# Kernel tuning notes

Hardware: AMD Instinct MI355X
Metric: run time of the kernel (lower is better)

The kernel has to match this reference:

```python
import jax, jax.numpy as jnp
import numpy as np

NTOKEN = 32000
NHID = 1024
BATCH = 64
LEAVES = 256          # leaves per balanced binary tree
SEQLEN = 768          # 3*LEAVES-2 = 766, padded to 768
MAX_DEPTH = 64        # stack bound; balanced tree needs ~log2(LEAVES)+2
OPEN, CLOSE = 0, 1
PAD = NTOKEN - 1


def _build_tree(rng, n_leaves):
    # "( left right )" encoding: open, subtrees, close; leaf ids in [2, NTOKEN-2]
    if n_leaves == 1:
        return [int(rng.integers(2, NTOKEN - 1))]
    l = n_leaves // 2
    return [OPEN] + _build_tree(rng, l) + _build_tree(rng, n_leaves - l) + [CLOSE]


def setup_inputs() -> dict:
    rng = np.random.default_rng(0)
    seqs = []
    for _ in range(BATCH):
        s = _build_tree(rng, LEAVES)
        s = s + [PAD] * (SEQLEN - len(s))
        seqs.append(s)
    tokens = jnp.asarray(np.asarray(seqs, dtype=np.int32).T)  # [S, B]

    key = jax.random.key(0)
    k1, k2 = jax.random.split(key, 2)
    emb = jax.random.normal(k1, (NTOKEN, NHID), jnp.float32) * 0.1
    emb = emb.at[PAD].set(0.0)  # padding_idx row is zero
    W = jax.random.normal(k2, (NHID, 2 * NHID), jnp.float32) * (1.0 / np.sqrt(2 * NHID))
    b = jnp.zeros((NHID,), jnp.float32)
    return {"tokens": tokens, "emb": emb, "W": W, "b": b}


def _parse_all(tokens, emb, W, b):
    # tokens: [S, B] int32. Shift-reduce stack machine, scanned over sequence,
    # vmapped over batch. Dropout is 0 (eval / default), so op = tanh(Linear).
    nhid = emb.shape[1]

    def parse_one(toks):  # toks: [S]
        stack0 = jnp.zeros((MAX_DEPTH, nhid), emb.dtype)

        def step(carry, idx):
            stack, ptr = carry
            is_close = idx == CLOSE
            is_open = idx == OPEN
            is_pad = idx == PAD
            left = stack[ptr - 2]
            right = stack[ptr - 1]
            combined = jnp.tanh(jnp.concatenate([left, right]) @ W.T + b)  # [nhid]
            leaf = emb[idx]
            push = jnp.where(is_close, combined, leaf)
            pos = jnp.where(is_close, ptr - 2, ptr)
            write = jnp.logical_not(is_open | is_pad)
            stack = stack.at[pos].set(jnp.where(write, push, stack[pos]))
            ptr = ptr + jnp.where(is_close, jnp.int32(-1),
                                  jnp.where(write, jnp.int32(1), jnp.int32(0)))
            return (stack, ptr), None

        (stack, _), _ = jax.lax.scan(step, (stack0, jnp.int32(0)), toks)
        return stack[0]  # root representation

    return jax.vmap(parse_one)(tokens.T)  # [B, nhid]


def reference(tokens, emb, W, b):
    return _parse_all(tokens, emb, W, b)
```

## Files before the change

kernel.cpp:

```cpp
#include <hip/hip_runtime.h>

#define B 64
#define SLEN 768
#define NHID 1024
#define K2 2048
#define NTOK 32000
#define PADTOK (NTOK-1)
#define MAXL 16
#define MAXN 256
#define NINT 256
#define STKD 14

typedef unsigned short u16;
typedef unsigned int u32;
typedef __attribute__((ext_vector_type(8))) short short8;
typedef __attribute__((ext_vector_type(4))) float f32x4;

__device__ __forceinline__ u16 f2b(float f) {
  union { float f; u32 i; } v; v.f = f;
  u32 x = v.i;
  return (u16)((x + 0x7FFFu + ((x >> 16) & 1u)) >> 16);
}
__device__ __forceinline__ float fast_tanh(float x) {
  float t = __expf(2.0f * x);
  return 1.0f - 2.0f / (t + 1.0f);
}
__device__ __forceinline__ void glds16(const void* g, void* l) {
  __builtin_amdgcn_global_load_lds(
      (const __attribute__((address_space(1))) void*)g,
      (__attribute__((address_space(3))) void*)l, 16, 0, 0);
}

__global__ void parse_wconv(const int* __restrict__ tokens,
                            const float* __restrict__ W,
                            int* __restrict__ cnt,
                            int* __restrict__ rootArr,
                            int* __restrict__ nNodes,
                            int* __restrict__ LeafTok,
                            int4* __restrict__ flat,
                            u16* __restrict__ Wbf) {
  if (blockIdx.x == 0) {
    int b = threadIdx.x;
    if (b >= B) return;
    int stk[STKD];
#pragma unroll
    for (int i = 0; i < STKD; ++i) stk[i] = 0;
    int nint = 0, leafc = 0;
    for (int t0 = 0; t0 < SLEN; t0 += 32) {
      int v[32];
#pragma unroll
      for (int i = 0; i < 32; ++i) v[i] = tokens[(t0 + i) * B + b];
#pragma unroll
      for (int i = 0; i < 32; ++i) {
        int idx = v[i];
        if (idx == 1) {
          int t1 = stk[0], t2 = stk[1];
          int l1 = (t1 >> 16) & 15, l2 = (t2 >> 16) & 15;
          int lvl = (l1 > l2 ? l1 : l2) + 1;
          if (lvl > 15) lvl = 15;
          if (nint < NINT)
            flat[b * NINT + nint] = make_int4(t2 & 0x4000FFFF, t1 & 0x4000FFFF, lvl, 0);
#pragma unroll
          for (int j = 1; j < STKD - 1; ++j) stk[j] = stk[j + 1];
          stk[0] = (lvl << 16) | nint;
          ++nint;
        } else if (idx != 0 && idx != PADTOK) {
          int slot = (leafc < 256) ? leafc : 255;
          LeafTok[b * 256 + slot] = idx;
          ++leafc;
#pragma unroll
          for (int j = STKD - 1; j > 0; --j) stk[j] = stk[j - 1];
          stk[0] = 0x40000000 | slot;
        }
      }
    }
    rootArr[b] = stk[0] & 0x4000FFFF;
    nNodes[b] = (nint < NINT) ? nint : NINT;
    cnt[b * MAXL + 0] = (leafc < 256) ? leafc : 256;
  } else {
    int id = (blockIdx.x - 1) * 256 + threadIdx.x;
    int stride = (gridDim.x - 1) * 256;
    for (int i = id; i < (NHID * K2) / 4; i += stride) {
      float4 v = reinterpret_cast<const float4*>(W)[i];
      ushort4 o = {f2b(v.x), f2b(v.y), f2b(v.z), f2b(v.w)};
      reinterpret_cast<ushort4*>(Wbf)[i] = o;
    }
  }
}

__global__ void bucket_leaf(const float* __restrict__ emb,
                            const int* __restrict__ LeafTok,
                            int* __restrict__ cnt,
                            const int* __restrict__ nNodes,
                            const int4* __restrict__ flat,
                            int4* __restrict__ nodes,
                            u16* __restrict__ LeafVals) {
  int bid = blockIdx.x;
  if (bid < B) {
    int i = threadIdx.x;
    if (i < nNodes[bid]) {
      int4 r = flat[bid * NINT + i];
      int slot = atomicAdd(&cnt[bid * MAXL + r.z], 1);
      if (slot < MAXN)
        nodes[((size_t)(bid * MAXL + r.z)) * MAXN + slot] = make_int4(r.x, r.y, i, 0);
    }
  } else {
    int r = bid - B;
    int b = r >> 8, slot = r & 255;
    if (slot < cnt[b * MAXL + 0]) {
      int tok = LeafTok[b * 256 + slot];
      const float* src = emb + (size_t)tok * NHID;
      u16* dst = LeafVals + ((size_t)(b * 256 + slot)) * NHID;
      int t = threadIdx.x * 4;
      float4 v = *reinterpret_cast<const float4*>(src + t);
      ushort4 o = {f2b(v.x), f2b(v.y), f2b(v.z), f2b(v.w)};
      *reinterpret_cast<ushort4*>(dst + t) = o;
    }
  }
}

__launch_bounds__(256, 3)
__global__ void combine_mfma(const u16* __restrict__ Wbf,
                             const float* __restrict__ bias,
                             const int* __restrict__ cnt,
                             const int4* __restrict__ nodes,
                             const int* __restrict__ rootArr,
                             const u16* __restrict__ LeafVals,
                             u16* __restrict__ Vals,
                             float* __restrict__ out,
                             int level) {
  __shared__ short As[8192];
  __shared__ short Bs[8192];
  __shared__ const u16* sL[128];
  __shared__ const u16* sR[128];
  __shared__ int sOut[128];
  __shared__ int sRoot[128];

  int cnt0 = cnt[level];
  if (cnt0 <= 0) return;
  int rowsTotal = B * cnt0;
  int mTiles = (rowsTotal + 127) >> 7;
  int totalTiles = mTiles * 8;
  int tid = threadIdx.x;
  int lane = tid & 63, wave = tid >> 6;
  int wm = wave & 1, wn = wave >> 1;

  for (int tile = blockIdx.x; tile < totalTiles; tile += gridDim.x) {
    int mt = tile >> 3, nt = tile & 7;
    int m0 = mt << 7, n0 = nt << 7;
    __syncthreads();
    if (tid < 128) {
      int r = m0 + tid;
      const u16* lp = Wbf; const u16* rp = Wbf; int ov = -1, rf = -1;
      if (r < rowsTotal) {
        int bb = r / cnt0, j = r - bb * cnt0;
        if (j < cnt[bb * MAXL + level]) {
          int4 rec = nodes[((size_t)(bb * MAXL + level)) * MAXN + j];
          int lr = rec.x, rr = rec.y;
          lp = (lr & 0x40000000) ? LeafVals + (size_t)(bb * 256 + (lr & 0xFFFF)) * NHID
                                 : Vals + ((size_t)bb * NINT + lr) * NHID;
          rp = (rr & 0x40000000) ? LeafVals + (size_t)(bb * 256 + (rr & 0xFFFF)) * NHID
                                 : Vals + ((size_t)bb * NINT + rr) * NHID;
          ov = bb * NINT + rec.z;
          int rt = rootArr[bb];
          if (!(rt & 0x40000000) && rec.z == rt) rf = bb * NHID;
        }
      }
      sL[tid] = lp; sR[tid] = rp; sOut[tid] = ov; sRoot[tid] = rf;
    }
    __syncthreads();

    int kq = (tid & 3) * 8;
    const u16* a0L = sL[tid >> 2] + kq;      const u16* a0R = sR[tid >> 2] + kq;
    const u16* a1L = sL[64 + (tid >> 2)] + kq; const u16* a1R = sR[64 + (tid >> 2)] + kq;
    const u16* b0 = Wbf + (size_t)(n0 + (tid >> 2)) * K2 + kq;
    const u16* b1 = Wbf + (size_t)(n0 + 64 + (tid >> 2)) * K2 + kq;
    short* AsW = As + wave * 512;
    short* BsW = Bs + wave * 512;

    f32x4 acc[4][4];
#pragma unroll
    for (int i = 0; i < 4; ++i)
#pragma unroll
      for (int j = 0; j < 4; ++j) acc[i][j] = {0.f, 0.f, 0.f, 0.f};

    int aBase = (wm * 64 + (lane & 15)) * 32 + (lane >> 4) * 8;
    int bBase = (wn * 64 + (lane & 15)) * 32 + (lane >> 4) * 8;

    for (int k0 = 0; k0 < K2; k0 += 64) {
#pragma unroll
      for (int p = 0; p < 2; ++p) {
        int k = k0 + p * 32;
        const u16* sa0 = (k < NHID) ? (a0L + k) : (a0R + (k - NHID));
        const u16* sa1 = (k < NHID) ? (a1L + k) : (a1R + (k - NHID));
        glds16(sa0, AsW + p * 4096);
        glds16(sa1, AsW + p * 4096 + 2048);
        glds16(b0 + k, BsW + p * 4096);
        glds16(b1 + k, BsW + p * 4096 + 2048);
      }
      __syncthreads();
#pragma unroll
      for (int p = 0; p < 2; ++p) {
        short8 af[4], bw[4];
#pragma unroll
        for (int mi = 0; mi < 4; ++mi)
          af[mi] = *reinterpret_cast<const short8*>(As + p * 4096 + aBase + mi * 512);
#pragma unroll
        for (int ni = 0; ni < 4; ++ni)
          bw[ni] = *reinterpret_cast<const short8*>(Bs + p * 4096 + bBase + ni * 512);
#pragma unroll
        for (int mi = 0; mi < 4; ++mi)
#pragma unroll
          for (int ni = 0; ni < 4; ++ni)
            acc[mi][ni] = __builtin_amdgcn_mfma_f32_16x16x32_bf16(
                af[mi], bw[ni], acc[mi][ni], 0, 0, 0);
      }
      __syncthreads();
    }

#pragma unroll
    for (int ni = 0; ni < 4; ++ni) {
      int n = n0 + wn * 64 + ni * 16 + (lane & 15);
      float bv = bias[n];
#pragma unroll
      for (int mi = 0; mi < 4; ++mi) {
#pragma unroll
        for (int reg = 0; reg < 4; ++reg) {
          int mloc = wm * 64 + mi * 16 + (lane >> 4) * 4 + reg;
          int ov = sOut[mloc];
          if (ov >= 0) {
            float v = fast_tanh(acc[mi][ni][reg] + bv);
            Vals[(size_t)ov * NHID + n] = f2b(v);
            int rf = sRoot[mloc];
            if (rf >= 0) out[rf + n] = v;
          }
        }
      }
    }
  }
}

extern "C" void kernel_launch(void* const* d_in, const int* in_sizes, int n_in,
                              void* d_out, int out_size, void* d_ws, size_t ws_size,
                              hipStream_t stream) {
  const int* tokens = (const int*)d_in[0];
  const float* emb  = (const float*)d_in[1];
  const float* W    = (const float*)d_in[2];
  const float* bias = (const float*)d_in[3];
  float* out = (float*)d_out;

  char* ws = (char*)d_ws;
  int* cnt      = (int*)ws;
  int* rootArr  = (int*)(ws + 4096);
  int* nNodes   = (int*)(ws + 4352);
  int* LeafTok  = (int*)(ws + 8192);
  int4* flat    = (int4*)(ws + 73728);
  int4* nodes   = (int4*)(ws + 335872);
  u16* Wbf      = (u16*)(ws + 4530176);
  u16* LeafVals = (u16*)(ws + 8724480);
  u16* Vals     = (u16*)(ws + 42278912);

  hipMemsetAsync(cnt, 0, 4096, stream);
  parse_wconv<<<65, 256, 0, stream>>>(tokens, W, cnt, rootArr, nNodes,
                                      LeafTok, flat, Wbf);
  bucket_leaf<<<B + B * 256, 256, 0, stream>>>(emb, LeafTok, cnt, nNodes,
                                               flat, nodes, LeafVals);
  for (int L = 1; L <= 9; ++L) {
    int expRows = B * (L <= 8 ? (256 >> L) : 1);
    int mT = (expRows + 127) / 128;
    int grid = mT * 8;
    combine_mfma<<<grid, 256, 0, stream>>>(Wbf, bias, cnt, nodes, rootArr,
                                           LeafVals, Vals, out, L);
  }
}
```

Baseline: 721.2 us.

## Bucket nodes by level during serial parse, drop memset and atomic bucketing pass

```diff
diff --git a/kernel.cpp b/kernel.cpp
--- a/kernel.cpp
+++ b/kernel.cpp
@@ -9,10 +9,10 @@
 #define MAXL 16
 #define MAXN 256
 #define NINT 256
-#define STKD 14
 
 typedef unsigned short u16;
 typedef unsigned int u32;
+typedef unsigned long long u64;
 typedef __attribute__((ext_vector_type(8))) short short8;
 typedef __attribute__((ext_vector_type(4))) float f32x4;
 
@@ -31,52 +31,62 @@
       (__attribute__((address_space(3))) void*)l, 16, 0, 0);
 }
 
+#define PUSH(NEW) do { s11=s10;s10=s9;s9=s8;s8=s7;s7=s6;s6=s5;s5=s4;s4=s3;s3=s2;s2=s1;s1=s0;s0=(NEW); } while(0)
+#define POP2PUSH(NEW) do { s0=(NEW);s1=s2;s2=s3;s3=s4;s4=s5;s5=s6;s6=s7;s7=s8;s8=s9;s9=s10;s10=s11; } while(0)
+
 __global__ void parse_wconv(const int* __restrict__ tokens,
                             const float* __restrict__ W,
                             int* __restrict__ cnt,
                             int* __restrict__ rootArr,
-                            int* __restrict__ nNodes,
                             int* __restrict__ LeafTok,
-                            int4* __restrict__ flat,
+                            int4* __restrict__ nodes,
                             u16* __restrict__ Wbf) {
   if (blockIdx.x == 0) {
     int b = threadIdx.x;
     if (b >= B) return;
-    int stk[STKD];
-#pragma unroll
-    for (int i = 0; i < STKD; ++i) stk[i] = 0;
+    int s0=0,s1=0,s2=0,s3=0,s4=0,s5=0,s6=0,s7=0,s8=0,s9=0,s10=0,s11=0;
+    u64 cA = 0, cB = 0;
     int nint = 0, leafc = 0;
-    for (int t0 = 0; t0 < SLEN; t0 += 32) {
-      int v[32];
-#pragma unroll
-      for (int i = 0; i < 32; ++i) v[i] = tokens[(t0 + i) * B + b];
-#pragma unroll
-      for (int i = 0; i < 32; ++i) {
+    for (int t0 = 0; t0 < SLEN; t0 += 16) {
+      int v[16];
+#pragma unroll
+      for (int i = 0; i < 16; ++i) v[i] = tokens[(t0 + i) * B + b];
+#pragma unroll
+      for (int i = 0; i < 16; ++i) {
         int idx = v[i];
         if (idx == 1) {
-          int t1 = stk[0], t2 = stk[1];
-          int l1 = (t1 >> 16) & 15, l2 = (t2 >> 16) & 15;
+          int l1 = (s0 >> 16) & 15, l2 = (s1 >> 16) & 15;
           int lvl = (l1 > l2 ? l1 : l2) + 1;
           if (lvl > 15) lvl = 15;
+          int slot;
+          if (lvl <= 8) {
+            int sh = (lvl - 1) * 8;
+            slot = (int)((cA >> sh) & 0xFF); cA += 1ull << sh;
+          } else {
+            int sh = (lvl - 9) * 8;
+            slot = (int)((cB >> sh) & 0xFF); cB += 1ull << sh;
+          }
           if (nint < NINT)
-            flat[b * NINT + nint] = make_int4(t2 & 0x4000FFFF, t1 & 0x4000FFFF, lvl, 0);
-#pragma unroll
-          for (int j = 1; j < STKD - 1; ++j) stk[j] = stk[j + 1];
-          stk[0] = (lvl << 16) | nint;
+            nodes[((size_t)(b * MAXL + lvl)) * MAXN + slot] =
+                make_int4(s1 & 0x4000FFFF, s0 & 0x4000FFFF, nint, 0);
+          POP2PUSH((lvl << 16) | nint);
           ++nint;
         } else if (idx != 0 && idx != PADTOK) {
           int slot = (leafc < 256) ? leafc : 255;
           LeafTok[b * 256 + slot] = idx;
           ++leafc;
-#pragma unroll
-          for (int j = STKD - 1; j > 0; --j) stk[j] = stk[j - 1];
-          stk[0] = 0x40000000 | slot;
+          PUSH(0x40000000 | slot);
         }
       }
     }
-    rootArr[b] = stk[0] & 0x4000FFFF;
-    nNodes[b] = (nint < NINT) ? nint : NINT;
+    rootArr[b] = s0 & 0x4000FFFF;
     cnt[b * MAXL + 0] = (leafc < 256) ? leafc : 256;
+#pragma unroll
+    for (int lvl = 1; lvl <= 8; ++lvl)
+      cnt[b * MAXL + lvl] = (int)((cA >> ((lvl - 1) * 8)) & 0xFF);
+#pragma unroll
+    for (int lvl = 9; lvl <= 15; ++lvl)
+      cnt[b * MAXL + lvl] = (int)((cB >> ((lvl - 9) * 8)) & 0xFF);
   } else {
     int id = (blockIdx.x - 1) * 256 + threadIdx.x;
     int stride = (gridDim.x - 1) * 256;
@@ -88,35 +98,20 @@
   }
 }
 
-__global__ void bucket_leaf(const float* __restrict__ emb,
+__global__ void leaf_gather(const float* __restrict__ emb,
                             const int* __restrict__ LeafTok,
-                            int* __restrict__ cnt,
-                            const int* __restrict__ nNodes,
-                            const int4* __restrict__ flat,
-                            int4* __restrict__ nodes,
+                            const int* __restrict__ cnt,
                             u16* __restrict__ LeafVals) {
-  int bid = blockIdx.x;
-  if (bid < B) {
-    int i = threadIdx.x;
-    if (i < nNodes[bid]) {
-      int4 r = flat[bid * NINT + i];
-      int slot = atomicAdd(&cnt[bid * MAXL + r.z], 1);
-      if (slot < MAXN)
-        nodes[((size_t)(bid * MAXL + r.z)) * MAXN + slot] = make_int4(r.x, r.y, i, 0);
-    }
-  } else {
-    int r = bid - B;
-    int b = r >> 8, slot = r & 255;
-    if (slot < cnt[b * MAXL + 0]) {
-      int tok = LeafTok[b * 256 + slot];
-      const float* src = emb + (size_t)tok * NHID;
-      u16* dst = LeafVals + ((size_t)(b * 256 + slot)) * NHID;
-      int t = threadIdx.x * 4;
-      float4 v = *reinterpret_cast<const float4*>(src + t);
-      ushort4 o = {f2b(v.x), f2b(v.y), f2b(v.z), f2b(v.w)};
-      *reinterpret_cast<ushort4*>(dst + t) = o;
-    }
-  }
+  int r = blockIdx.x;
+  int b = r >> 8, slot = r & 255;
+  if (slot >= cnt[b * MAXL + 0]) return;
+  int tok = LeafTok[b * 256 + slot];
+  const float* src = emb + (size_t)tok * NHID;
+  u16* dst = LeafVals + ((size_t)(b * 256 + slot)) * NHID;
+  int t = threadIdx.x * 4;
+  float4 v = *reinterpret_cast<const float4*>(src + t);
+  ushort4 o = {f2b(v.x), f2b(v.y), f2b(v.z), f2b(v.w)};
+  *reinterpret_cast<ushort4*>(dst + t) = o;
 }
 
 __launch_bounds__(256, 3)
@@ -171,7 +166,7 @@
     __syncthreads();
 
     int kq = (tid & 3) * 8;
-    const u16* a0L = sL[tid >> 2] + kq;      const u16* a0R = sR[tid >> 2] + kq;
+    const u16* a0L = sL[tid >> 2] + kq;        const u16* a0R = sR[tid >> 2] + kq;
     const u16* a1L = sL[64 + (tid >> 2)] + kq; const u16* a1R = sR[64 + (tid >> 2)] + kq;
     const u16* b0 = Wbf + (size_t)(n0 + (tid >> 2)) * K2 + kq;
     const u16* b1 = Wbf + (size_t)(n0 + 64 + (tid >> 2)) * K2 + kq;
@@ -252,19 +247,15 @@
   char* ws = (char*)d_ws;
   int* cnt      = (int*)ws;
   int* rootArr  = (int*)(ws + 4096);
-  int* nNodes   = (int*)(ws + 4352);
   int* LeafTok  = (int*)(ws + 8192);
-  int4* flat    = (int4*)(ws + 73728);
-  int4* nodes   = (int4*)(ws + 335872);
-  u16* Wbf      = (u16*)(ws + 4530176);
-  u16* LeafVals = (u16*)(ws + 8724480);
-  u16* Vals     = (u16*)(ws + 42278912);
-
-  hipMemsetAsync(cnt, 0, 4096, stream);
-  parse_wconv<<<65, 256, 0, stream>>>(tokens, W, cnt, rootArr, nNodes,
-                                      LeafTok, flat, Wbf);
-  bucket_leaf<<<B + B * 256, 256, 0, stream>>>(emb, LeafTok, cnt, nNodes,
-                                               flat, nodes, LeafVals);
+  int4* nodes   = (int4*)(ws + 73728);
+  u16* Wbf      = (u16*)(ws + 4268032);
+  u16* LeafVals = (u16*)(ws + 8462336);
+  u16* Vals     = (u16*)(ws + 42016768);
+
+  parse_wconv<<<257, 256, 0, stream>>>(tokens, W, cnt, rootArr, LeafTok,
+                                       nodes, Wbf);
+  leaf_gather<<<B * 256, 256, 0, stream>>>(emb, LeafTok, cnt, LeafVals);
   for (int L = 1; L <= 9; ++L) {
     int expRows = B * (L <= 8 ? (256 >> L) : 1);
     int mT = (expRows + 127) / 128;
```

New measurement: 738.0 us. 2.3% more time.
